# Optimization experiments

Measured on AMD Instinct MI355X. Metric: run time of the kernel, lower is better.

Reference implementation:

```python
import jax, jax.numpy as jnp
import numpy as np

HIDDEN = 2048
HEADS = 16
HEAD_DIM = HIDDEN // HEADS  # 128
NUM_LATENTS = 16
LN_EPS = 1e-5


def setup_inputs() -> dict:
    key = jax.random.key(0)
    ks = jax.random.split(key, 16)
    B, S, D = 8, 4096, HIDDEN
    glorot = lambda k, fi, fo: jax.random.uniform(k, (fi, fo), jnp.float32,
                                                  -np.sqrt(6.0 / (fi + fo)), np.sqrt(6.0 / (fi + fo)))
    return {
        "hidden_states": jax.random.normal(ks[0], (B, S, D), jnp.float32),
        "ln_g": jnp.ones((D,), jnp.float32),
        "ln_b": jnp.zeros((D,), jnp.float32),
        "latents": 0.02 * jax.random.normal(ks[1], (NUM_LATENTS, D), jnp.float32),
        # weights stored as [in, out] (transpose of torch Linear.weight)
        "w_lq": glorot(ks[2], D, D), "b_lq": jnp.zeros((D,), jnp.float32),
        "w_k": glorot(ks[3], D, D), "b_k": jnp.zeros((D,), jnp.float32),
        "w_v": glorot(ks[4], D, D), "b_v": jnp.zeros((D,), jnp.float32),
        "w_lv": glorot(ks[5], D, D), "b_lv": jnp.zeros((D,), jnp.float32),
        "w_out": glorot(ks[6], D, D), "b_out": jnp.zeros((D,), jnp.float32),
    }


def reference(hidden_states, ln_g, ln_b, latents, w_lq, b_lq, w_k, b_k,
              w_v, b_v, w_lv, b_lv, w_out, b_out):
    x = hidden_states
    B, S, D = x.shape
    H, hd, L = HEADS, HEAD_DIM, latents.shape[0]
    # pre-LayerNorm
    mu = jnp.mean(x, axis=-1, keepdims=True)
    var = jnp.var(x, axis=-1, keepdims=True)
    h = (x - mu) / jnp.sqrt(var + LN_EPS) * ln_g + ln_b
    # projections
    k = (h @ w_k + b_k).reshape(B, S, H, hd)          # keys   [B,S,H,hd]
    v = (h @ w_v + b_v).reshape(B, S, H, hd)          # values [B,S,H,hd]
    q = (latents @ w_lq + b_lq).reshape(L, H, hd)     # latent queries [L,H,hd]
    # latent cross-attention: scores [B,H,L,S]
    scores = jnp.einsum("lhd,bshd->bhls", q, k) / np.sqrt(hd).astype(x.dtype)
    probs = jax.nn.softmax(scores, axis=-1)           # dropout is identity at eval
    ctx = jnp.einsum("bhls,bshd->blhd", probs, v).reshape(B, L, D)
    lv = ctx @ w_lv + b_lv                            # [B,L,D]
    pooled = jnp.mean(lv, axis=1, keepdims=True)      # [B,1,D]
    out = pooled @ w_out + b_out                      # [B,1,D]
    return x + jnp.broadcast_to(out, (B, S, D))       # residual add
```

## Files before the change

kernel.cpp:

```cpp
#include <hip/hip_runtime.h>
#include <hip/hip_bf16.h>

#define BB 8
#define SS 4096
#define DD 2048
#define HH 16
#define HDIM 128
#define LL 16
#define JJ 256
#define ROWS (BB*SS)
#define LN_EPS 1e-5f

typedef __attribute__((ext_vector_type(8))) short short8;
typedef __attribute__((ext_vector_type(4))) float f32x4;

typedef __attribute__((address_space(1))) const unsigned int gu32;
typedef __attribute__((address_space(3))) unsigned int lu32;
__device__ __forceinline__ void async16(const void* g, void* l) {
  __builtin_amdgcn_global_load_lds((gu32*)g, (lu32*)l, 16, 0, 0);
}

__device__ __forceinline__ unsigned short f2bf(float f) {
  unsigned int u = __builtin_bit_cast(unsigned int, f);
  u += 0x7fffu + ((u >> 16) & 1u);
  return (unsigned short)(u >> 16);
}
__device__ __forceinline__ float bf2f(unsigned short u) {
  unsigned int v = ((unsigned int)u) << 16;
  return __builtin_bit_cast(float, v);
}

__global__ __launch_bounds__(256) void k_q_part(const float* latents, const float* w_lq, float* qpart) {
  int c  = blockIdx.x * 256 + threadIdx.x;
  int e0 = blockIdx.y * 64;
  float acc[16];
#pragma unroll
  for (int l = 0; l < 16; ++l) acc[l] = 0.f;
  for (int e = e0; e < e0 + 64; ++e) {
    float w = w_lq[(size_t)e * 2048 + c];
#pragma unroll
    for (int l = 0; l < 16; ++l) acc[l] += latents[l * 2048 + e] * w;
  }
#pragma unroll
  for (int l = 0; l < 16; ++l) qpart[((size_t)blockIdx.y * 16 + l) * 2048 + c] = acc[l];
}

__global__ __launch_bounds__(256) void k_reduce(const float* part, const float* bias, float* out, int R) {
  int c = blockIdx.x * 256 + threadIdx.x;
  int r = blockIdx.y;
  float s = bias[c];
  for (int p = 0; p < 32; ++p) s += part[((size_t)p * R + r) * 2048 + c];
  out[r * 2048 + c] = s;
}

__global__ __launch_bounds__(256) void k_lnT(const float* x, const float* ln_g, const float* ln_b,
                                             short* h) {
  int row = blockIdx.x;
  int t = threadIdx.x;
  const float4* xr = (const float4*)(x + (size_t)row * 2048);
  float4 v0 = xr[t * 2];
  float4 v1 = xr[t * 2 + 1];
  float s  = v0.x + v0.y + v0.z + v0.w + v1.x + v1.y + v1.z + v1.w;
  float s2 = v0.x*v0.x + v0.y*v0.y + v0.z*v0.z + v0.w*v0.w
           + v1.x*v1.x + v1.y*v1.y + v1.z*v1.z + v1.w*v1.w;
#pragma unroll
  for (int o = 32; o; o >>= 1) { s += __shfl_down(s, o); s2 += __shfl_down(s2, o); }
  __shared__ float red[8];
  int wid = t >> 6;
  if ((t & 63) == 0) { red[wid] = s; red[4 + wid] = s2; }
  __syncthreads();
  float ts  = red[0] + red[1] + red[2] + red[3];
  float ts2 = red[4] + red[5] + red[6] + red[7];
  float mu   = ts * (1.0f / 2048.0f);
  float var  = ts2 * (1.0f / 2048.0f) - mu * mu;
  float rstd = rsqrtf(var + LN_EPS);
  const float4* gp = (const float4*)ln_g;
  const float4* bp = (const float4*)ln_b;
  float4 g0 = gp[t * 2], g1 = gp[t * 2 + 1];
  float4 b0 = bp[t * 2], b1 = bp[t * 2 + 1];
  short8 o;
  o[0] = (short)f2bf((v0.x - mu) * rstd * g0.x + b0.x);
  o[1] = (short)f2bf((v0.y - mu) * rstd * g0.y + b0.y);
  o[2] = (short)f2bf((v0.z - mu) * rstd * g0.z + b0.z);
  o[3] = (short)f2bf((v0.w - mu) * rstd * g0.w + b0.w);
  o[4] = (short)f2bf((v1.x - mu) * rstd * g1.x + b1.x);
  o[5] = (short)f2bf((v1.y - mu) * rstd * g1.y + b1.y);
  o[6] = (short)f2bf((v1.z - mu) * rstd * g1.z + b1.z);
  o[7] = (short)f2bf((v1.w - mu) * rstd * g1.w + b1.w);
  ((short8*)(h + (size_t)row * 2048))[t] = o;
}

__global__ __launch_bounds__(256) void k_wq(const float* w_k, const float* q, short* wq_t) {
  int e = blockIdx.x;
  __shared__ float wrow[2048];
  for (int i = threadIdx.x; i < 512; i += 256)
    ((float4*)wrow)[i] = ((const float4*)(w_k + (size_t)e * 2048))[i];
  __syncthreads();
  int j = threadIdx.x;
  int h = j >> 4, l = j & 15;
  const float* qrow = q + l * 2048 + h * 128;
  const float* wr = wrow + h * 128;
  float acc = 0.f;
#pragma unroll 8
  for (int d = 0; d < 128; ++d) acc += wr[d] * qrow[d];
  wq_t[(size_t)j * 2048 + e] = (short)f2bf(acc * 0.08838834764831845f);
}

__global__ __launch_bounds__(256, 2) void k_scores(const short* h, const short* wq_t, float* scores) {
  int s0 = blockIdx.x * 256;
  int j0 = blockIdx.y * 64;
  int b  = blockIdx.z;
  __shared__ short lds[2 * 4096 + 2 * 16384];
  int t = threadIdx.x, lane = t & 63, w = t >> 6;
  f32x4 zero = {0.f, 0.f, 0.f, 0.f};
  f32x4 acc[4][4];
#pragma unroll
  for (int m = 0; m < 4; ++m)
#pragma unroll
    for (int n = 0; n < 4; ++n) acc[m][n] = zero;

  int rsel = t >> 3;
  int kcs  = (t & 7) ^ ((t >> 3) & 7);
  const short* hbase  = h + ((size_t)(b * 4096 + s0)) * 2048;
  const short* wqbase = wq_t + (size_t)j0 * 2048;
  int koff0 = (((lane >> 4)) ^ (lane & 7)) * 8;
  int koff1 = ((4 + (lane >> 4)) ^ (lane & 7)) * 8;

  int cur = 0;
  {
    short* lA = lds;
    short* lB = lds + 8192;
#pragma unroll
    for (int i = 0; i < 8; ++i)
      async16(hbase + (size_t)(i * 32 + rsel) * 2048 + kcs * 8,
              lB + (i * 256 + w * 64) * 8);
#pragma unroll
    for (int i = 0; i < 2; ++i)
      async16(wqbase + (size_t)(i * 32 + rsel) * 2048 + kcs * 8,
              lA + (i * 256 + w * 64) * 8);
  }

  for (int it = 0; it < 32; ++it) {
    if (it < 31) {
      int k0 = (it + 1) * 64;
      short* lA1 = lds + (cur ^ 1) * 4096;
      short* lB1 = lds + 8192 + (cur ^ 1) * 16384;
#pragma unroll
      for (int i = 0; i < 8; ++i)
        async16(hbase + (size_t)(i * 32 + rsel) * 2048 + k0 + kcs * 8,
                lB1 + (i * 256 + w * 64) * 8);
#pragma unroll
      for (int i = 0; i < 2; ++i)
        async16(wqbase + (size_t)(i * 32 + rsel) * 2048 + k0 + kcs * 8,
                lA1 + (i * 256 + w * 64) * 8);
      asm volatile("s_waitcnt vmcnt(10)" ::: "memory");
    } else {
      asm volatile("s_waitcnt vmcnt(0)" ::: "memory");
    }
    __builtin_amdgcn_s_barrier();
    __builtin_amdgcn_sched_barrier(0);
    const short* lA = lds + cur * 4096;
    const short* lB = lds + 8192 + cur * 16384;
#pragma unroll
    for (int kk = 0; kk < 2; ++kk) {
      int ko = kk ? koff1 : koff0;
      short8 afr[4];
#pragma unroll
      for (int m = 0; m < 4; ++m)
        afr[m] = *(const short8*)(lA + (m * 16 + (lane & 15)) * 64 + ko);
#pragma unroll
      for (int n = 0; n < 4; ++n) {
        short8 bfr = *(const short8*)(lB + (w * 64 + n * 16 + (lane & 15)) * 64 + ko);
#pragma unroll
        for (int m = 0; m < 4; ++m)
          acc[m][n] = __builtin_amdgcn_mfma_f32_16x16x32_bf16(afr[m], bfr, acc[m][n], 0, 0, 0);
      }
    }
    __builtin_amdgcn_s_barrier();
    cur ^= 1;
  }

  int r4 = (lane >> 4) * 4, cc = lane & 15;
#pragma unroll
  for (int m = 0; m < 4; ++m) {
    int j = j0 + m * 16 + r4;
#pragma unroll
    for (int n = 0; n < 4; ++n) {
      int s = s0 + w * 64 + n * 16 + cc;
      float* dst = scores + ((size_t)b * 256 + j) * 4096 + s;
#pragma unroll
      for (int i = 0; i < 4; ++i) dst[(size_t)i * 4096] = acc[m][n][i];
    }
  }
}

__global__ __launch_bounds__(256) void k_smax_a(const float* scores, float* msum) {
  int j = blockIdx.x, b = blockIdx.y;
  const float* row = scores + ((size_t)b * 256 + j) * 4096;
  float v[16];
  float mx = -1e30f;
#pragma unroll
  for (int i = 0; i < 16; ++i) { v[i] = row[threadIdx.x + 256 * i]; mx = fmaxf(mx, v[i]); }
#pragma unroll
  for (int o = 32; o; o >>= 1) mx = fmaxf(mx, __shfl_xor(mx, o));
  __shared__ float redm[4], reds[4];
  if ((threadIdx.x & 63) == 0) redm[threadIdx.x >> 6] = mx;
  __syncthreads();
  mx = fmaxf(fmaxf(redm[0], redm[1]), fmaxf(redm[2], redm[3]));
  float sum = 0.f;
#pragma unroll
  for (int i = 0; i < 16; ++i) sum += __expf(v[i] - mx);
#pragma unroll
  for (int o = 32; o; o >>= 1) sum += __shfl_xor(sum, o);
  if ((threadIdx.x & 63) == 0) reds[threadIdx.x >> 6] = sum;
  __syncthreads();
  if (threadIdx.x == 0) {
    sum = reds[0] + reds[1] + reds[2] + reds[3];
    msum[(b * 256 + j) * 2]     = mx;
    msum[(b * 256 + j) * 2 + 1] = 1.0f / (16.0f * sum);
  }
}

__global__ __launch_bounds__(256) void k_smax_b(const float* scores, const float* msum, float* pbar) {
  int b = blockIdx.y, sc = blockIdx.x;
  int t = threadIdx.x, lane = t & 63, jq = t >> 6;
  int s = sc * 64 + lane;
  const float* srow = scores + ((size_t)(b * 256 + jq * 64)) * 4096 + s;
  const float* ms = msum + (b * 256 + jq * 64) * 2;
  float acc[4] = {0.f, 0.f, 0.f, 0.f};
  for (int jj = 0; jj < 64; ++jj) {
    float m  = ms[jj * 2];
    float iv = ms[jj * 2 + 1];
    float v = __expf(srow[(size_t)jj * 4096] - m) * iv;
    acc[jj >> 4] += v;
  }
#pragma unroll
  for (int r = 0; r < 4; ++r)
    pbar[((size_t)b * 16 + jq * 4 + r) * 4096 + s] = acc[r];
}

__global__ __launch_bounds__(256) void k_tbar2(const short* h, const float* pbar, float* Tpart) {
  int ec = blockIdx.x;
  int sp = blockIdx.y;
  int b  = blockIdx.z;
  int t  = threadIdx.x;
  int e0 = ec * 1024 + t * 4;
  __shared__ float lp[16 * 128];
  {
    int hh = t >> 4, so = (t & 15) * 8;
    const float4* src = (const float4*)(pbar + ((size_t)b * 16 + hh) * 4096 + sp * 128 + so);
    float4* dst = (float4*)(lp + hh * 128 + so);
    dst[0] = src[0]; dst[1] = src[1];
  }
  __syncthreads();
  f32x4 acc[16];
#pragma unroll
  for (int hh = 0; hh < 16; ++hh) acc[hh] = (f32x4){0.f, 0.f, 0.f, 0.f};

  const short* hbase = h + ((size_t)(b * 4096 + sp * 128)) * 2048 + e0;
  for (int si = 0; si < 128; si += 4) {
    float hv[4][4];
#pragma unroll
    for (int r = 0; r < 4; ++r) {
      short4 hh4 = *(const short4*)(hbase + (size_t)(si + r) * 2048);
      hv[r][0] = bf2f((unsigned short)hh4.x);
      hv[r][1] = bf2f((unsigned short)hh4.y);
      hv[r][2] = bf2f((unsigned short)hh4.z);
      hv[r][3] = bf2f((unsigned short)hh4.w);
    }
#pragma unroll
    for (int hh = 0; hh < 16; ++hh) {
      float4 ph = *(const float4*)(lp + hh * 128 + si);
#pragma unroll
      for (int c = 0; c < 4; ++c)
        acc[hh][c] += ph.x * hv[0][c] + ph.y * hv[1][c] + ph.z * hv[2][c] + ph.w * hv[3][c];
    }
  }
#pragma unroll
  for (int hh = 0; hh < 16; ++hh)
    *(f32x4*)(Tpart + ((size_t)((sp * 8 + b) * 16 + hh)) * 2048 + e0) = acc[hh];
}

__global__ __launch_bounds__(256) void k_tred(const float* Tpart, float* Tbar) {
  int bh = blockIdx.x;
  for (int e = threadIdx.x; e < 2048; e += 256) {
    float s = 0.f;
#pragma unroll
    for (int p = 0; p < 32; ++p) s += Tpart[((size_t)p * 128 + bh) * 2048 + e];
    Tbar[(size_t)bh * 2048 + e] = s;
  }
}

__global__ __launch_bounds__(256) void k_cbar_part(const float* Tbar, const float* w_v, float* part) {
  int c  = blockIdx.x * 256 + threadIdx.x;
  int e0 = blockIdx.y * 64;
  int h  = c >> 7;
  float acc[8];
#pragma unroll
  for (int b = 0; b < 8; ++b) acc[b] = 0.f;
  for (int e = e0; e < e0 + 64; ++e) {
    float wv = w_v[(size_t)e * 2048 + c];
#pragma unroll
    for (int b = 0; b < 8; ++b) acc[b] += Tbar[((size_t)b * 16 + h) * 2048 + e] * wv;
  }
#pragma unroll
  for (int b = 0; b < 8; ++b) part[((size_t)blockIdx.y * 8 + b) * 2048 + c] = acc[b];
}

__global__ __launch_bounds__(256) void k_vecmat_part(const float* vin, const float* W, float* part) {
  int c  = blockIdx.x * 256 + threadIdx.x;
  int e0 = blockIdx.y * 64;
  float acc[8];
#pragma unroll
  for (int b = 0; b < 8; ++b) acc[b] = 0.f;
  for (int e = e0; e < e0 + 64; ++e) {
    float wv = W[(size_t)e * 2048 + c];
#pragma unroll
    for (int b = 0; b < 8; ++b) acc[b] += vin[b * 2048 + e] * wv;
  }
#pragma unroll
  for (int b = 0; b < 8; ++b) part[((size_t)blockIdx.y * 8 + b) * 2048 + c] = acc[b];
}

__global__ __launch_bounds__(256) void k_resid(const float* x, const float* outv, float* out) {
  size_t i4 = (size_t)blockIdx.x * 256 + threadIdx.x;
  size_t total4 = (size_t)ROWS * 512;
  size_t stride = (size_t)gridDim.x * 256;
  for (; i4 < total4; i4 += stride) {
    int b  = (int)(i4 >> 21);
    int c4 = (int)(i4 & 511);
    float4 xv = ((const float4*)x)[i4];
    float4 ov = ((const float4*)outv)[b * 512 + c4];
    float4 o;
    o.x = xv.x + ov.x; o.y = xv.y + ov.y;
    o.z = xv.z + ov.z; o.w = xv.w + ov.w;
    ((float4*)out)[i4] = o;
  }
}

extern "C" void kernel_launch(void* const* d_in, const int* in_sizes, int n_in,
                              void* d_out, int out_size, void* d_ws, size_t ws_size,
                              hipStream_t stream) {
  const float* x       = (const float*)d_in[0];
  const float* ln_g    = (const float*)d_in[1];
  const float* ln_b    = (const float*)d_in[2];
  const float* latents = (const float*)d_in[3];
  const float* w_lq    = (const float*)d_in[4];
  const float* b_lq    = (const float*)d_in[5];
  const float* w_k     = (const float*)d_in[6];
  const float* w_v     = (const float*)d_in[8];
  const float* b_v     = (const float*)d_in[9];
  const float* w_lv    = (const float*)d_in[10];
  const float* b_lv    = (const float*)d_in[11];
  const float* w_out   = (const float*)d_in[12];
  const float* b_out   = (const float*)d_in[13];

  char* base = (char*)d_out;
  float* scores = (float*)(base);
  short* h      = (short*)(base + 33554432);
  float* Tpart  = (float*)(base + 167772160);
  float* pbar   = (float*)(base + 201326592);
  float* msum   = (float*)(base + 203423744);
  float* q      = (float*)(base + 203440128);
  short* wq_t   = (short*)(base + 203571200);
  float* Tbar   = (float*)(base + 204619776);
  float* cbar   = (float*)(base + 205144064);
  float* pooled = (float*)(base + 205209600);
  float* part   = (float*)(base + 205275136);
  float* outv   = (float*)d_ws;
  float* out    = (float*)d_out;

  k_q_part     <<<dim3(8, 32), 256, 0, stream>>>(latents, w_lq, part);
  k_reduce     <<<dim3(8, 16), 256, 0, stream>>>(part, b_lq, q, 16);
  k_lnT        <<<32768, 256, 0, stream>>>(x, ln_g, ln_b, h);
  k_wq         <<<2048, 256, 0, stream>>>(w_k, q, wq_t);
  k_scores     <<<dim3(16, 4, 8), 256, 0, stream>>>(h, wq_t, scores);
  k_smax_a     <<<dim3(256, 8), 256, 0, stream>>>(scores, msum);
  k_smax_b     <<<dim3(64, 8), 256, 0, stream>>>(scores, msum, pbar);
  k_tbar2      <<<dim3(2, 32, 8), 256, 0, stream>>>(h, pbar, Tpart);
  k_tred       <<<128, 256, 0, stream>>>(Tpart, Tbar);
  k_cbar_part  <<<dim3(8, 32), 256, 0, stream>>>(Tbar, w_v, part);
  k_reduce     <<<dim3(8, 8), 256, 0, stream>>>(part, b_v, cbar, 8);
  k_vecmat_part<<<dim3(8, 32), 256, 0, stream>>>(cbar, w_lv, part);
  k_reduce     <<<dim3(8, 8), 256, 0, stream>>>(part, b_lv, pooled, 8);
  k_vecmat_part<<<dim3(8, 32), 256, 0, stream>>>(pooled, w_out, part);
  k_reduce     <<<dim3(8, 8), 256, 0, stream>>>(part, b_out, outv, 8);
  k_resid      <<<2048, 256, 0, stream>>>(x, outv, out);
}
```

Baseline: 476.7 us.

## Fuse softmax statistics into scores epilogue and merge prob-reduce with T accumulation

The scores GEMM now writes bf16 scores and computes per-block partial max/sum-exp in its epilogue, replacing the separate row-stats kernel with a small merge kernel. The second softmax pass and the pbar-times-h reduction are merged into one kernel that stages a score tile in LDS, builds the head-averaged probabilities, and accumulates T with 8-wide loads. This removes a full fp32 scores round trip and a kernel launch, at the cost of bf16 rounding of the scores and a kernel launched with only 256 blocks and a large register footprint.

```diff
diff --git a/kernel.cpp b/kernel.cpp
--- a/kernel.cpp
+++ b/kernel.cpp
@@ -106,7 +106,8 @@
   wq_t[(size_t)j * 2048 + e] = (short)f2bf(acc * 0.08838834764831845f);
 }
 
-__global__ __launch_bounds__(256, 2) void k_scores(const short* h, const short* wq_t, float* scores) {
+__global__ __launch_bounds__(256, 2) void k_scores(const short* h, const short* wq_t,
+                                                   short* scores, float* part_ms) {
   int s0 = blockIdx.x * 256;
   int j0 = blockIdx.y * 64;
   int b  = blockIdx.z;
@@ -180,110 +181,112 @@
     cur ^= 1;
   }
 
-  int r4 = (lane >> 4) * 4, cc = lane & 15;
+  int hi = lane >> 4, cc = lane & 15;
+  __syncthreads();
+  float2* msred = (float2*)lds;
 #pragma unroll
   for (int m = 0; m < 4; ++m) {
-    int j = j0 + m * 16 + r4;
-#pragma unroll
-    for (int n = 0; n < 4; ++n) {
-      int s = s0 + w * 64 + n * 16 + cc;
-      float* dst = scores + ((size_t)b * 256 + j) * 4096 + s;
-#pragma unroll
-      for (int i = 0; i < 4; ++i) dst[(size_t)i * 4096] = acc[m][n][i];
-    }
-  }
-}
-
-__global__ __launch_bounds__(256) void k_smax_a(const float* scores, float* msum) {
-  int j = blockIdx.x, b = blockIdx.y;
-  const float* row = scores + ((size_t)b * 256 + j) * 4096;
-  float v[16];
-  float mx = -1e30f;
-#pragma unroll
-  for (int i = 0; i < 16; ++i) { v[i] = row[threadIdx.x + 256 * i]; mx = fmaxf(mx, v[i]); }
-#pragma unroll
-  for (int o = 32; o; o >>= 1) mx = fmaxf(mx, __shfl_xor(mx, o));
-  __shared__ float redm[4], reds[4];
-  if ((threadIdx.x & 63) == 0) redm[threadIdx.x >> 6] = mx;
-  __syncthreads();
-  mx = fmaxf(fmaxf(redm[0], redm[1]), fmaxf(redm[2], redm[3]));
-  float sum = 0.f;
-#pragma unroll
-  for (int i = 0; i < 16; ++i) sum += __expf(v[i] - mx);
-#pragma unroll
-  for (int o = 32; o; o >>= 1) sum += __shfl_xor(sum, o);
-  if ((threadIdx.x & 63) == 0) reds[threadIdx.x >> 6] = sum;
-  __syncthreads();
-  if (threadIdx.x == 0) {
-    sum = reds[0] + reds[1] + reds[2] + reds[3];
-    msum[(b * 256 + j) * 2]     = mx;
-    msum[(b * 256 + j) * 2 + 1] = 1.0f / (16.0f * sum);
-  }
-}
-
-__global__ __launch_bounds__(256) void k_smax_b(const float* scores, const float* msum, float* pbar) {
-  int b = blockIdx.y, sc = blockIdx.x;
-  int t = threadIdx.x, lane = t & 63, jq = t >> 6;
-  int s = sc * 64 + lane;
-  const float* srow = scores + ((size_t)(b * 256 + jq * 64)) * 4096 + s;
-  const float* ms = msum + (b * 256 + jq * 64) * 2;
-  float acc[4] = {0.f, 0.f, 0.f, 0.f};
-  for (int jj = 0; jj < 64; ++jj) {
-    float m  = ms[jj * 2];
-    float iv = ms[jj * 2 + 1];
-    float v = __expf(srow[(size_t)jj * 4096] - m) * iv;
-    acc[jj >> 4] += v;
-  }
-#pragma unroll
-  for (int r = 0; r < 4; ++r)
-    pbar[((size_t)b * 16 + jq * 4 + r) * 4096 + s] = acc[r];
-}
-
-__global__ __launch_bounds__(256) void k_tbar2(const short* h, const float* pbar, float* Tpart) {
-  int ec = blockIdx.x;
-  int sp = blockIdx.y;
-  int b  = blockIdx.z;
+#pragma unroll
+    for (int i = 0; i < 4; ++i) {
+      int j = j0 + m * 16 + hi * 4 + i;
+      float v[4];
+#pragma unroll
+      for (int n = 0; n < 4; ++n) {
+        unsigned short u = f2bf(acc[m][n][i]);
+        scores[((size_t)(b * 256 + j)) * 4096 + s0 + w * 64 + n * 16 + cc] = (short)u;
+        v[n] = bf2f(u);
+      }
+      float mx = fmaxf(fmaxf(v[0], v[1]), fmaxf(v[2], v[3]));
+#pragma unroll
+      for (int o = 1; o < 16; o <<= 1) mx = fmaxf(mx, __shfl_xor(mx, o));
+      float sm = __expf(v[0] - mx) + __expf(v[1] - mx) + __expf(v[2] - mx) + __expf(v[3] - mx);
+#pragma unroll
+      for (int o = 1; o < 16; o <<= 1) sm += __shfl_xor(sm, o);
+      if (cc == 0) msred[(m * 16 + hi * 4 + i) * 4 + w] = make_float2(mx, sm);
+    }
+  }
+  __syncthreads();
+  if (t < 64) {
+    float2 p0 = msred[t * 4 + 0], p1 = msred[t * 4 + 1];
+    float2 p2 = msred[t * 4 + 2], p3 = msred[t * 4 + 3];
+    float M = fmaxf(fmaxf(p0.x, p1.x), fmaxf(p2.x, p3.x));
+    float S = p0.y * __expf(p0.x - M) + p1.y * __expf(p1.x - M)
+            + p2.y * __expf(p2.x - M) + p3.y * __expf(p3.x - M);
+    ((float2*)part_ms)[((size_t)(b * 256 + j0 + t)) * 16 + blockIdx.x] = make_float2(M, S);
+  }
+}
+
+__global__ __launch_bounds__(256) void k_msum(const float* part_ms, float* msum) {
+  int row = blockIdx.x * 256 + threadIdx.x;
+  const float2* p = (const float2*)(part_ms + (size_t)row * 32);
+  float2 v[16];
+  float M = -1e30f;
+#pragma unroll
+  for (int i = 0; i < 16; ++i) { v[i] = p[i]; M = fmaxf(M, v[i].x); }
+  float S = 0.f;
+#pragma unroll
+  for (int i = 0; i < 16; ++i) S += v[i].y * __expf(v[i].x - M);
+  msum[row * 2]     = M;
+  msum[row * 2 + 1] = 1.0f / (16.0f * S);
+}
+
+__global__ __launch_bounds__(256) void k_pt(const short* scores, const float* msum,
+                                            const short* h, float* Tpart) {
+  int sp = blockIdx.x;
+  int b  = blockIdx.y;
   int t  = threadIdx.x;
-  int e0 = ec * 1024 + t * 4;
+  __shared__ short sc[256 * 128];
   __shared__ float lp[16 * 128];
+#pragma unroll
+  for (int rr = 0; rr < 2; ++rr) {
+    int j = rr * 128 + (t >> 1);
+    const short8* src = (const short8*)(scores + ((size_t)(b * 256 + j)) * 4096 + sp * 128 + (t & 1) * 64);
+    short8* dst = (short8*)(sc + j * 128 + (t & 1) * 64);
+#pragma unroll
+    for (int i = 0; i < 8; ++i) dst[i] = src[i];
+  }
+  __syncthreads();
   {
-    int hh = t >> 4, so = (t & 15) * 8;
-    const float4* src = (const float4*)(pbar + ((size_t)b * 16 + hh) * 4096 + sp * 128 + so);
-    float4* dst = (float4*)(lp + hh * 128 + so);
-    dst[0] = src[0]; dst[1] = src[1];
-  }
-  __syncthreads();
-  f32x4 acc[16];
-#pragma unroll
-  for (int hh = 0; hh < 16; ++hh) acc[hh] = (f32x4){0.f, 0.f, 0.f, 0.f};
-
-  const short* hbase = h + ((size_t)(b * 4096 + sp * 128)) * 2048 + e0;
-  for (int si = 0; si < 128; si += 4) {
-    float hv[4][4];
-#pragma unroll
-    for (int r = 0; r < 4; ++r) {
-      short4 hh4 = *(const short4*)(hbase + (size_t)(si + r) * 2048);
-      hv[r][0] = bf2f((unsigned short)hh4.x);
-      hv[r][1] = bf2f((unsigned short)hh4.y);
-      hv[r][2] = bf2f((unsigned short)hh4.z);
-      hv[r][3] = bf2f((unsigned short)hh4.w);
-    }
+    int s = t & 127, hg = (t >> 7) * 8;
+    for (int hh = hg; hh < hg + 8; ++hh) {
+      const float* ms = msum + (b * 256 + hh * 16) * 2;
+      float accp = 0.f;
+#pragma unroll
+      for (int l = 0; l < 16; ++l)
+        accp += __expf(bf2f((unsigned short)sc[(hh * 16 + l) * 128 + s]) - ms[l * 2]) * ms[l * 2 + 1];
+      lp[hh * 128 + s] = accp;
+    }
+  }
+  __syncthreads();
+  f32x4 a0[16], a1[16];
+#pragma unroll
+  for (int hh = 0; hh < 16; ++hh) { a0[hh] = (f32x4){0,0,0,0}; a1[hh] = (f32x4){0,0,0,0}; }
+  const short* hb = h + ((size_t)(b * 4096 + sp * 128)) * 2048 + t * 8;
+  for (int si = 0; si < 128; ++si) {
+    short8 hv8 = *(const short8*)(hb + (size_t)si * 2048);
+    float hv[8];
+#pragma unroll
+    for (int c = 0; c < 8; ++c) hv[c] = bf2f((unsigned short)hv8[c]);
 #pragma unroll
     for (int hh = 0; hh < 16; ++hh) {
-      float4 ph = *(const float4*)(lp + hh * 128 + si);
-#pragma unroll
-      for (int c = 0; c < 4; ++c)
-        acc[hh][c] += ph.x * hv[0][c] + ph.y * hv[1][c] + ph.z * hv[2][c] + ph.w * hv[3][c];
-    }
-  }
-#pragma unroll
-  for (int hh = 0; hh < 16; ++hh)
-    *(f32x4*)(Tpart + ((size_t)((sp * 8 + b) * 16 + hh)) * 2048 + e0) = acc[hh];
+      float p = lp[hh * 128 + si];
+#pragma unroll
+      for (int c = 0; c < 4; ++c) { a0[hh][c] += p * hv[c]; a1[hh][c] += p * hv[4 + c]; }
+    }
+  }
+#pragma unroll
+  for (int hh = 0; hh < 16; ++hh) {
+    float* dst = Tpart + ((size_t)(sp * 128 + b * 16 + hh)) * 2048 + t * 8;
+    *(f32x4*)dst = a0[hh];
+    *(f32x4*)(dst + 4) = a1[hh];
+  }
 }
 
 __global__ __launch_bounds__(256) void k_tred(const float* Tpart, float* Tbar) {
   int bh = blockIdx.x;
-  for (int e = threadIdx.x; e < 2048; e += 256) {
+  int e  = blockIdx.y * 1024 + threadIdx.x;
+#pragma unroll
+  for (int k = 0; k < 4; ++k, e += 256) {
     float s = 0.f;
 #pragma unroll
     for (int p = 0; p < 32; ++p) s += Tpart[((size_t)p * 128 + bh) * 2048 + e];
@@ -356,29 +359,28 @@
   const float* b_out   = (const float*)d_in[13];
 
   char* base = (char*)d_out;
-  float* scores = (float*)(base);
-  short* h      = (short*)(base + 33554432);
-  float* Tpart  = (float*)(base + 167772160);
-  float* pbar   = (float*)(base + 201326592);
-  float* msum   = (float*)(base + 203423744);
-  float* q      = (float*)(base + 203440128);
-  short* wq_t   = (short*)(base + 203571200);
-  float* Tbar   = (float*)(base + 204619776);
-  float* cbar   = (float*)(base + 205144064);
-  float* pooled = (float*)(base + 205209600);
-  float* part   = (float*)(base + 205275136);
-  float* outv   = (float*)d_ws;
-  float* out    = (float*)d_out;
+  short* scores  = (short*)(base);
+  short* h       = (short*)(base + 16777216);
+  float* Tpart   = (float*)(base + 150994944);
+  float* part_ms = (float*)(base + 184549376);
+  float* msum    = (float*)(base + 184811520);
+  float* q       = (float*)(base + 184827904);
+  short* wq_t    = (short*)(base + 184958976);
+  float* Tbar    = (float*)(base + 186007552);
+  float* cbar    = (float*)(base + 186531840);
+  float* pooled  = (float*)(base + 186597376);
+  float* part    = (float*)(base + 186662912);
+  float* outv    = (float*)d_ws;
+  float* out     = (float*)d_out;
 
   k_q_part     <<<dim3(8, 32), 256, 0, stream>>>(latents, w_lq, part);
   k_reduce     <<<dim3(8, 16), 256, 0, stream>>>(part, b_lq, q, 16);
   k_lnT        <<<32768, 256, 0, stream>>>(x, ln_g, ln_b, h);
   k_wq         <<<2048, 256, 0, stream>>>(w_k, q, wq_t);
-  k_scores     <<<dim3(16, 4, 8), 256, 0, stream>>>(h, wq_t, scores);
-  k_smax_a     <<<dim3(256, 8), 256, 0, stream>>>(scores, msum);
-  k_smax_b     <<<dim3(64, 8), 256, 0, stream>>>(scores, msum, pbar);
-  k_tbar2      <<<dim3(2, 32, 8), 256, 0, stream>>>(h, pbar, Tpart);
-  k_tred       <<<128, 256, 0, stream>>>(Tpart, Tbar);
+  k_scores     <<<dim3(16, 4, 8), 256, 0, stream>>>(h, wq_t, scores, part_ms);
+  k_msum       <<<8, 256, 0, stream>>>(part_ms, msum);
+  k_pt         <<<dim3(32, 8), 256, 0, stream>>>(scores, msum, h, Tpart);
+  k_tred       <<<dim3(128, 2), 256, 0, stream>>>(Tpart, Tbar);
   k_cbar_part  <<<dim3(8, 32), 256, 0, stream>>>(Tbar, w_v, part);
   k_reduce     <<<dim3(8, 8), 256, 0, stream>>>(part, b_v, cbar, 8);
   k_vecmat_part<<<dim3(8, 32), 256, 0, stream>>>(cbar, w_lv, part);
```

Result: faster. 451.3 us (-5.3%).
